# Optimization experiments

Hardware: AMD Instinct MI355X
Metric: run time of the kernel (lower is better)

Reference implementation:

```python
import jax, jax.numpy as jnp
import numpy as np

MIN_NORM = 1e-15
BALL_EPS_F32 = 0.004  # BALL_EPS[torch.float32]


def _norm(x):
    return jnp.maximum(jnp.linalg.norm(x, axis=-1, keepdims=True), MIN_NORM)


def project(x, c=1.0):
    norm = _norm(x)
    maxnorm = (1.0 - BALL_EPS_F32) / (c ** 0.5)
    return jnp.where(norm > maxnorm, x / norm * maxnorm, x)


def expmap0(u, c=1.0):
    sqrt_c = c ** 0.5
    un = _norm(u)
    gamma = jnp.tanh(jnp.clip(sqrt_c * un, -15.0, 15.0)) * u / (sqrt_c * un)
    return project(gamma, c)


def artanh(x):
    x = jnp.clip(x, -1.0 + 1e-5, 1.0 - 1e-5)
    return 0.5 * (jnp.log1p(x) - jnp.log1p(-x))


def logmap0(y, c=1.0):
    sqrt_c = c ** 0.5
    yn = _norm(y)
    return y / yn / sqrt_c * artanh(sqrt_c * yn)


def mobius_add(x, y, c=1.0):
    x2 = jnp.sum(x * x, axis=-1, keepdims=True)
    y2 = jnp.sum(y * y, axis=-1, keepdims=True)
    xy = jnp.sum(x * y, axis=-1, keepdims=True)
    num = (1 + 2 * c * xy + c * y2) * x + (1 - c * x2) * y
    denom = 1 + 2 * c * xy + (c ** 2) * x2 * y2
    return num / jnp.maximum(denom, MIN_NORM)


def p_exp_map(v):
    nv = jnp.maximum(jnp.linalg.norm(v, axis=-1, keepdims=True), 1e-10)
    return jnp.tanh(nv) * v / nv


def setup_inputs() -> dict:
    key = jax.random.key(0)
    ks = jax.random.split(key, 16)
    E, N, B = 1_000_000, 100_000, 512
    n_rel, D, A = 200, 64, 5
    R = 2 * n_rel + 1  # 401

    q_sub = jax.random.randint(ks[0], (B,), 0, N, dtype=jnp.int32)
    q_rel = jax.random.randint(ks[1], (B,), 0, R, dtype=jnp.int32)
    hidden = jax.random.normal(ks[2], (N, D), dtype=jnp.float32)

    r_idx = jax.random.randint(ks[3], (E,), 0, B, dtype=jnp.int32)
    rel = jax.random.randint(ks[4], (E,), 0, R, dtype=jnp.int32)
    sub = jax.random.randint(ks[5], (E,), 0, N, dtype=jnp.int32)
    obj = jax.random.randint(ks[6], (E,), 0, N, dtype=jnp.int32)
    dummy = jnp.zeros((E,), dtype=jnp.int32)
    edges = jnp.stack([r_idx, dummy, rel, dummy, sub, obj], axis=1)  # [E,6]

    s = 1.0 / np.sqrt(D)
    sa = 1.0 / np.sqrt(A)
    rela_embed = jax.random.normal(ks[7], (R, D), dtype=jnp.float32)
    query_embed = jax.random.normal(ks[8], (R, D), dtype=jnp.float32)
    Ws = jax.random.uniform(ks[9], (A, D), jnp.float32, -s, s)
    Wr = jax.random.uniform(ks[10], (A, D), jnp.float32, -s, s)
    Wqr_w = jax.random.uniform(ks[11], (A, D), jnp.float32, -s, s)
    Wqr_b = jax.random.uniform(ks[12], (A,), jnp.float32, -s, s)
    walpha_w = jax.random.uniform(ks[13], (1, A), jnp.float32, -sa, sa)
    walpha_b = jax.random.uniform(ks[14], (1,), jnp.float32, -sa, sa)
    Wh = jax.random.uniform(ks[15], (D, D), jnp.float32, -s, s)

    return {
        "q_sub": q_sub, "q_rel": q_rel, "hidden": hidden, "edges": edges,
        "n_node": N, "old_nodes_new_idx": jax.random.randint(jax.random.fold_in(key, 99), (100,), 0, N, dtype=jnp.int32),
        "rela_embed": rela_embed, "query_embed": query_embed,
        "Ws": Ws, "Wr": Wr, "Wqr_w": Wqr_w, "Wqr_b": Wqr_b,
        "walpha_w": walpha_w, "walpha_b": walpha_b, "Wh": Wh,
    }


def reference(q_sub, q_rel, hidden, edges, n_node, old_nodes_new_idx,
              rela_embed, query_embed, Ws, Wr, Wqr_w, Wqr_b,
              walpha_w, walpha_b, Wh):
    sub = edges[:, 4]
    rel = edges[:, 2]
    obj = edges[:, 5]
    r_idx = edges[:, 0]

    hs = hidden[sub]                     # [E, D] gather
    hr = rela_embed[rel]                 # [E, D]
    h_qr = query_embed[q_rel][r_idx]     # [E, D]

    # attention (note: bilinear/non_linear branch in the original is dead code)
    pre = hs @ Ws.T + hr @ Wr.T + (h_qr @ Wqr_w.T + Wqr_b)   # [E, A]
    alpha = jax.nn.sigmoid(jax.nn.relu(pre) @ walpha_w.T + walpha_b)  # [E, 1]

    hr_h = expmap0(hr, 1.0)
    hs_h = expmap0(hs, 1.0)
    message = logmap0(project(mobius_add(hs_h, hr_h, 1.0), 1.0), 1.0)
    message = alpha * message            # [E, D]

    message_agg = jax.ops.segment_sum(message, obj, num_segments=n_node)  # [N, D]
    a = message_agg @ Wh.T
    a = p_exp_map(a)
    hidden_new = logmap0(a, 1.0)         # act is identity
    return hidden_new
```

## Files before the change

kernel.cpp:

```cpp
#include <hip/hip_runtime.h>
#include <hip/hip_bf16.h>
#include <hip/hip_fp16.h>


__device__ __forceinline__ float wave_sum(float v) {
#pragma unroll
    for (int off = 32; off > 0; off >>= 1) v += __shfl_xor(v, off, 64);
    return v;
}

__device__ __forceinline__ float frcp(float x) {
#if __has_builtin(__builtin_amdgcn_rcpf)
    return __builtin_amdgcn_rcpf(x);
#else
    return 1.f / x;
#endif
}
__device__ __forceinline__ float fsqrt_(float x) {
#if __has_builtin(__builtin_amdgcn_sqrtf)
    return __builtin_amdgcn_sqrtf(x);
#else
    return sqrtf(x);
#endif
}
__device__ __forceinline__ float flog2_(float x) {
#if __has_builtin(__builtin_amdgcn_logf)
    return __builtin_amdgcn_logf(x);
#else
    return log2f(x);
#endif
}
__device__ __forceinline__ float fexp2_(float x) {
#if __has_builtin(__builtin_amdgcn_exp2f)
    return __builtin_amdgcn_exp2f(x);
#else
    return exp2f(x);
#endif
}

__device__ __forceinline__ unsigned pk2(float a, float b) {
    __half2 h = __floats2half2_rn(a, b);
    return __builtin_bit_cast(unsigned, h);
}
__device__ __forceinline__ float2 upk2(unsigned u) {
    __half2 h = __builtin_bit_cast(__half2, u);
    return __half22float2(h);
}

__device__ __forceinline__ void expmap0_scale(float norm, float& s, float& x2) {
    const float maxn = 1.0f - 0.004f;
    float un = fmaxf(norm, 1e-15f);
    float th = tanhf(fminf(un, 15.0f));
    float gs = th / un;
    float ng = gs * norm;
    float ps = ng > maxn ? maxn / ng : 1.0f;
    s = gs * ps;
    float sn = s * norm;
    x2 = sn * sn;
}


__global__ void prep_fused16(const int* __restrict__ q_rel,
                             const float* __restrict__ query_embed,
                             const float* __restrict__ Wqr_w,
                             const float* __restrict__ Wqr_b,
                             const float* __restrict__ rela_embed,
                             const float* __restrict__ Wr,
                             const float* __restrict__ hidden,
                             const float* __restrict__ Ws,
                             __half* __restrict__ hidden16,
                             uint4* __restrict__ hs_aux16,
                             __half* __restrict__ hr_h16,
                             uint4* __restrict__ hr_aux16,
                             uint4* __restrict__ preq16,
                             __half* __restrict__ agg16,
                             int N, int R, int B) {
    int wid = (blockIdx.x * blockDim.x + threadIdx.x) >> 6;
    int lane = threadIdx.x & 63;
    int nwaves = (N + 3) >> 2;
    if (wid < nwaves) {
        int q = lane >> 4, j = lane & 15;
        int n = wid * 4 + q;
        bool act = n < N;
        int nc = act ? n : N - 1;

        float4 u = *(const float4*)(hidden + (size_t)nc * 64 + 4 * j);
        float4 w0 = *(const float4*)(Ws + 0 * 64 + 4 * j);
        float4 w1 = *(const float4*)(Ws + 1 * 64 + 4 * j);
        float4 w2 = *(const float4*)(Ws + 2 * 64 + 4 * j);
        float4 w3 = *(const float4*)(Ws + 3 * 64 + 4 * j);
        float4 w4 = *(const float4*)(Ws + 4 * 64 + 4 * j);

#define DOT4(a, b) (fmaf((a).x, (b).x, fmaf((a).y, (b).y, fmaf((a).z, (b).z, (a).w * (b).w))))
        float p0 = DOT4(u, u);
        float p1 = DOT4(u, w0);
        float p2 = DOT4(u, w1);
        float p3 = DOT4(u, w2);
        float p4 = DOT4(u, w3);
        float p5 = DOT4(u, w4);
#undef DOT4
#pragma unroll
        for (int off = 1; off < 16; off <<= 1) {
            p0 += __shfl_xor(p0, off, 64);
            p1 += __shfl_xor(p1, off, 64);
            p2 += __shfl_xor(p2, off, 64);
            p3 += __shfl_xor(p3, off, 64);
            p4 += __shfl_xor(p4, off, 64);
            p5 += __shfl_xor(p5, off, 64);
        }
        float s, x2;
        expmap0_scale(fsqrt_(p0), s, x2);
        if (act) {
            uint2 hp; hp.x = pk2(u.x, u.y); hp.y = pk2(u.z, u.w);
            *(uint2*)(hidden16 + (size_t)n * 64 + 4 * j) = hp;
            uint2 zz; zz.x = 0u; zz.y = 0u;
            ((uint2*)(agg16 + (size_t)n * 64))[j] = zz;
            if (j == 0) {
                uint4 o; o.x = pk2(p1, p2); o.y = pk2(p3, p4); o.z = pk2(p5, 0.f); o.w = pk2(x2, s);
                hs_aux16[n] = o;
            }
        }
        return;
    }
    int w2 = wid - nwaves;
    if (w2 < R) {
        int r = w2;
        float u = rela_embed[r * 64 + lane];
        float p0 = u * u;
        float p1 = u * Wr[0 * 64 + lane];
        float p2 = u * Wr[1 * 64 + lane];
        float p3 = u * Wr[2 * 64 + lane];
        float p4 = u * Wr[3 * 64 + lane];
        float p5 = u * Wr[4 * 64 + lane];
#pragma unroll
        for (int off = 1; off < 64; off <<= 1) {
            p0 += __shfl_xor(p0, off, 64);
            p1 += __shfl_xor(p1, off, 64);
            p2 += __shfl_xor(p2, off, 64);
            p3 += __shfl_xor(p3, off, 64);
            p4 += __shfl_xor(p4, off, 64);
            p5 += __shfl_xor(p5, off, 64);
        }
        float s, y2;
        expmap0_scale(fsqrt_(p0), s, y2);
        hr_h16[r * 64 + lane] = __float2half(s * u);
        if (lane == 0) {
            uint4 o; o.x = pk2(p1, p2); o.y = pk2(p3, p4); o.z = pk2(p5, 0.f); o.w = pk2(y2, 0.f);
            hr_aux16[r] = o;
        }
    } else if (w2 < R + B) {
        int b = w2 - R;
        int qr = q_rel[b];
        float q = query_embed[qr * 64 + lane];
        float p1 = q * Wqr_w[0 * 64 + lane];
        float p2 = q * Wqr_w[1 * 64 + lane];
        float p3 = q * Wqr_w[2 * 64 + lane];
        float p4 = q * Wqr_w[3 * 64 + lane];
        float p5 = q * Wqr_w[4 * 64 + lane];
#pragma unroll
        for (int off = 1; off < 64; off <<= 1) {
            p1 += __shfl_xor(p1, off, 64);
            p2 += __shfl_xor(p2, off, 64);
            p3 += __shfl_xor(p3, off, 64);
            p4 += __shfl_xor(p4, off, 64);
            p5 += __shfl_xor(p5, off, 64);
        }
        if (lane == 0) {
            uint4 o;
            o.x = pk2(p1 + Wqr_b[0], p2 + Wqr_b[1]);
            o.y = pk2(p3 + Wqr_b[2], p4 + Wqr_b[3]);
            o.z = pk2(p5 + Wqr_b[4], 0.f);
            o.w = pk2(0.f, 0.f);
            preq16[b] = o;
        }
    }
}

__device__ __forceinline__ void edge_chain(
    unsigned hu_lo, unsigned hu_hi, unsigned yu_lo, unsigned yu_hi,
    uint4 hsa, uint4 hra, uint4 pqa,
    const float* wa, float wb,
    bool act, __half2* __restrict__ dst ) {
    float2 hs01 = upk2(hsa.x), hs23 = upk2(hsa.y), hs4 = upk2(hsa.z), hsxs = upk2(hsa.w);
    float2 hr01 = upk2(hra.x), hr23 = upk2(hra.y), hr4 = upk2(hra.z), hry = upk2(hra.w);
    float2 pq01 = upk2(pqa.x), pq23 = upk2(pqa.y), pq4 = upk2(pqa.z);
    float x2 = hsxs.x, s = hsxs.y, y2 = hry.x;

    float2 hl = upk2(hu_lo), hh = upk2(hu_hi);
    float2 yl = upk2(yu_lo), yh = upk2(yu_hi);

    float p = hl.x * yl.x;
    p = fmaf(hl.y, yl.y, p);
    p = fmaf(hh.x, yh.x, p);
    p = fmaf(hh.y, yh.y, p);
    p += __shfl_xor(p, 1, 64);
    p += __shfl_xor(p, 2, 64);
    p += __shfl_xor(p, 4, 64);
    p += __shfl_xor(p, 8, 64);
    float xy = p * s;

    float z = wb;
    z = fmaf(fmaxf(hs01.x + hr01.x + pq01.x, 0.f), wa[0], z);
    z = fmaf(fmaxf(hs01.y + hr01.y + pq01.y, 0.f), wa[1], z);
    z = fmaf(fmaxf(hs23.x + hr23.x + pq23.x, 0.f), wa[2], z);
    z = fmaf(fmaxf(hs23.y + hr23.y + pq23.y, 0.f), wa[3], z);
    z = fmaf(fmaxf(hs4.x + hr4.x + pq4.x, 0.f), wa[4], z);
    float alpha = frcp(1.f + fexp2_(z * -1.44269504f));

    float Af  = 1.f + 2.f * xy + y2;
    float Bf  = 1.f - x2;
    float den = fmaxf(1.f + 2.f * xy + x2 * y2, 1e-15f);
    float inv = frcp(den);
    float nm2 = fmaxf(fmaf(Af * Af, x2, fmaf(2.f * Af * Bf, xy, Bf * Bf * y2)), 0.f);
    float nm  = fsqrt_(nm2) * inv;
    const float maxn = 1.0f - 0.004f;
    float ps  = nm > maxn ? maxn * frcp(nm) : 1.f;
    float yn  = fmaxf(fminf(nm, maxn), 1e-15f);
    float ratio = (1.f + yn) * frcp(1.f - yn);
    float art = 0.34657359f * flog2_(ratio);
    float k  = inv * ps * alpha * art * frcp(yn);
    float cx = k * Af * s;
    float cy = k * Bf;

    __half2 q_lo = __floats2half2_rn(fmaf(cx, hl.x, cy * yl.x), fmaf(cx, hl.y, cy * yl.y));
    __half2 q_hi = __floats2half2_rn(fmaf(cx, hh.x, cy * yh.x), fmaf(cx, hh.y, cy * yh.y));
    if (act) {
        unsafeAtomicAdd(dst, q_lo);
        unsafeAtomicAdd(dst + 16, q_hi);
    }
}

__global__ __launch_bounds__(256) void edge_kernel8c(
    const int* __restrict__ edges,
    const __half* __restrict__ hidden16,
    const __half* __restrict__ hr_h16,
    const uint4* __restrict__ hs_aux16,
    const uint4* __restrict__ hr_aux16,
    const uint4* __restrict__ preq16,
    const float* __restrict__ walpha_w,
    const float* __restrict__ walpha_b,
    __half2* __restrict__ agg,
    int E)
{
    int wid = (blockIdx.x * blockDim.x + threadIdx.x) >> 6;
    int lane = threadIdx.x & 63;
    int g = lane >> 4;
    int j = lane & 15;

    int e0 = wid * 8 + g;
    int e1 = wid * 8 + 4 + g;
    bool act0 = e0 < E, act1 = e1 < E;
    int ec0 = act0 ? e0 : E - 1;
    int ec1 = act1 ? e1 : E - 1;

    const long long* er0 = (const long long*)(edges + (size_t)ec0 * 6);
    const long long* er1 = (const long long*)(edges + (size_t)ec1 * 6);
    long long a0 = __builtin_nontemporal_load(er0);
    long long b0 = __builtin_nontemporal_load(er0 + 1);
    long long c0 = __builtin_nontemporal_load(er0 + 2);
    long long a1 = __builtin_nontemporal_load(er1);
    long long b1 = __builtin_nontemporal_load(er1 + 1);
    long long c1 = __builtin_nontemporal_load(er1 + 2);
    int r0 = (int)a0, rel0 = (int)b0, sub0 = (int)c0, obj0 = (int)(c0 >> 32);
    int r1 = (int)a1, rel1 = (int)b1, sub1 = (int)c1, obj1 = (int)(c1 >> 32);

    uint4 hsa0 = hs_aux16[sub0];
    uint4 hra0 = hr_aux16[rel0];
    uint4 pqa0 = preq16[r0];
    uint4 hsa1 = hs_aux16[sub1];
    uint4 hra1 = hr_aux16[rel1];
    uint4 pqa1 = preq16[r1];

    const unsigned* hrow0 = (const unsigned*)(hidden16 + (size_t)sub0 * 64);
    const unsigned* yrow0 = (const unsigned*)(hr_h16 + (size_t)rel0 * 64);
    const unsigned* hrow1 = (const unsigned*)(hidden16 + (size_t)sub1 * 64);
    const unsigned* yrow1 = (const unsigned*)(hr_h16 + (size_t)rel1 * 64);
    unsigned hu_lo0 = hrow0[j], hu_hi0 = hrow0[16 + j];
    unsigned yu_lo0 = yrow0[j], yu_hi0 = yrow0[16 + j];
    unsigned hu_lo1 = hrow1[j], hu_hi1 = hrow1[16 + j];
    unsigned yu_lo1 = yrow1[j], yu_hi1 = yrow1[16 + j];

    float wa[5];
    wa[0] = walpha_w[0]; wa[1] = walpha_w[1]; wa[2] = walpha_w[2];
    wa[3] = walpha_w[3]; wa[4] = walpha_w[4];
    float wb = walpha_b[0];

    edge_chain(hu_lo0, hu_hi0, yu_lo0, yu_hi0, hsa0, hra0, pqa0, wa, wb,
               act0, agg + (size_t)obj0 * 32 + j);
    edge_chain(hu_lo1, hu_hi1, yu_lo1, yu_hi1, hsa1, hra1, pqa1, wa, wb,
               act1, agg + (size_t)obj1 * 32 + j);
}

__global__ __launch_bounds__(256) void final_gemm16(
    float* __restrict__ out,
    const __half* __restrict__ agg16,
    const float* __restrict__ Wh,
    int N)
{
    __shared__ __half tile[64 * 64];
    int t = threadIdx.x;
    int lane = t & 63;
    int w = t >> 6;

    float wh[64];
    const float4* whr = (const float4*)(Wh + (size_t)lane * 64);
#pragma unroll
    for (int i = 0; i < 16; ++i) {
        float4 v = whr[i];
        wh[4 * i] = v.x; wh[4 * i + 1] = v.y; wh[4 * i + 2] = v.z; wh[4 * i + 3] = v.w;
    }

    int ntiles = (N + 63) >> 6;
    for (int ti = blockIdx.x; ti < ntiles; ti += gridDim.x) {
        int base = ti << 6;
        int nrow = min(64, N - base);
        __syncthreads();
        {
            const uint2* src = (const uint2*)(agg16 + (size_t)base * 64);
            uint2* dst = (uint2*)tile;
            int nu2 = nrow * 16;
            for (int i = t; i < nu2; i += 256) dst[i] = src[i];
        }
        __syncthreads();
#pragma unroll 1
        for (int r = 0; r < 16; ++r) {
            int n = base + w * 16 + r;
            if (n >= N) break;
            const uint2* arow = (const uint2*)(tile + (w * 16 + r) * 64);
            float acc = 0.f;
#pragma unroll
            for (int kk = 0; kk < 16; ++kk) {
                uint2 u = arow[kk];
                float2 f0 = upk2(u.x), f1 = upk2(u.y);
                acc = fmaf(f0.x, wh[4 * kk], acc);
                acc = fmaf(f0.y, wh[4 * kk + 1], acc);
                acc = fmaf(f1.x, wh[4 * kk + 2], acc);
                acc = fmaf(f1.y, wh[4 * kk + 3], acc);
            }
            float n2 = wave_sum(acc * acc);
            float na = fsqrt_(n2);
            float nv = fmaxf(na, 1e-10f);
            float pn = tanhf(nv);
            float rinv = frcp(nv);
            float pp = pn * acc * rinv;
            float np = pn * (na * rinv);
            float yn = fmaxf(np, 1e-15f);
            float tt = fminf(yn, 1.f - 1e-5f);
            float ratio = (1.f + tt) * frcp(1.f - tt);
            float art = 0.34657359f * flog2_(ratio);
            out[(size_t)n * 64 + lane] = pp * art * frcp(yn);
        }
    }
}


__global__ void prep_small_kernel(const int* __restrict__ q_rel,
                                  const float* __restrict__ query_embed,
                                  const float* __restrict__ Wqr_w,
                                  const float* __restrict__ Wqr_b,
                                  const float* __restrict__ rela_embed,
                                  const float* __restrict__ Wr,
                                  float* __restrict__ hr_h,
                                  float* __restrict__ hr_aux,
                                  float* __restrict__ preq,
                                  int R, int B, int A) {
    int w = (blockIdx.x * blockDim.x + threadIdx.x) >> 6;
    int lane = threadIdx.x & 63;
    if (w < R) {
        int r = w;
        float u = rela_embed[r * 64 + lane];
        float n2 = wave_sum(u * u);
        float s, y2;
        expmap0_scale(fsqrt_(n2), s, y2);
        hr_h[r * 64 + lane] = s * u;
        for (int a = 0; a < A; ++a) {
            float p = wave_sum(u * Wr[a * 64 + lane]);
            if (lane == 0) hr_aux[r * 8 + a] = p;
        }
        if (lane == 0) hr_aux[r * 8 + 6] = y2;
    } else if (w < R + B) {
        int b = w - R;
        int qr = q_rel[b];
        float q = query_embed[qr * 64 + lane];
        for (int a = 0; a < A; ++a) {
            float p = wave_sum(q * Wqr_w[a * 64 + lane]);
            if (lane == 0) preq[b * 8 + a] = p + Wqr_b[a];
        }
    }
}

__global__ void prep_node_kernel(const float* __restrict__ hidden,
                                 const float* __restrict__ Ws,
                                 float* __restrict__ hs_aux, int N, int A) {
    int w = (blockIdx.x * blockDim.x + threadIdx.x) >> 6;
    if (w >= N) return;
    int lane = threadIdx.x & 63;
    float u = hidden[(size_t)w * 64 + lane];
    float n2 = wave_sum(u * u);
    float s, x2;
    expmap0_scale(fsqrt_(n2), s, x2);
    for (int a = 0; a < A; ++a) {
        float p = wave_sum(u * Ws[a * 64 + lane]);
        if (lane == 0) hs_aux[w * 8 + a] = p;
    }
    if (lane == 0) { hs_aux[w * 8 + 6] = x2; hs_aux[w * 8 + 7] = s; }
}

__global__ void edge_kernel_f32(const int* __restrict__ edges,
                                const float* __restrict__ hidden,
                                const float* __restrict__ hr_h,
                                const float* __restrict__ hr_aux,
                                const float* __restrict__ hs_aux,
                                const float* __restrict__ preq,
                                const float* __restrict__ walpha_w,
                                const float* __restrict__ walpha_b,
                                float* __restrict__ agg,
                                int E, int A) {
    int w = (blockIdx.x * blockDim.x + threadIdx.x) >> 6;
    if (w >= E) return;
    int lane = threadIdx.x & 63;
    const int* er = edges + (size_t)w * 6;
    int r_idx = er[0], rel = er[2], sub = er[4], obj = er[5];

    float s  = hs_aux[(size_t)sub * 8 + 7];
    float x2 = hs_aux[(size_t)sub * 8 + 6];
    float h  = hidden[(size_t)sub * 64 + lane];
    float x  = h * s;
    float y  = hr_h[(size_t)rel * 64 + lane];
    float y2 = hr_aux[(size_t)rel * 8 + 6];
    float xy = wave_sum(x * y);

    float z = walpha_b[0];
    for (int a = 0; a < A; ++a) {
        float pre = hs_aux[(size_t)sub * 8 + a] + hr_aux[(size_t)rel * 8 + a] + preq[(size_t)r_idx * 8 + a];
        z += fmaxf(pre, 0.f) * walpha_w[a];
    }
    float alpha = frcp(1.f + fexp2_(z * -1.44269504f));

    float Af = 1.f + 2.f * xy + y2;
    float Bf = 1.f - x2;
    float den = fmaxf(1.f + 2.f * xy + x2 * y2, 1e-15f);
    float inv = frcp(den);
    float nm2 = fmaxf(Af * Af * x2 + 2.f * Af * Bf * xy + Bf * Bf * y2, 0.f);
    float nm = fsqrt_(nm2) * inv;
    const float maxn = 1.0f - 0.004f;
    float ps = nm > maxn ? maxn * frcp(nm) : 1.f;
    float yn = fmaxf(fminf(nm, maxn), 1e-15f);
    float ratio = (1.f + yn) * frcp(1.f - yn);
    float art = 0.34657359f * flog2_(ratio);
    float k = inv * ps * alpha * art * frcp(yn);
    float msg = fmaf(k * Af * s, h, k * Bf * y);
    unsafeAtomicAdd(agg + (size_t)obj * 64 + lane, msg);
}

__global__ void final_kernel_f32(float* __restrict__ out,
                                 const float* __restrict__ Wh,
                                 int N) {
    __shared__ float WhT[64 * 64];
    int t = threadIdx.x;
    for (int i = t; i < 64 * 64; i += blockDim.x) {
        int row = i >> 6, col = i & 63;
        WhT[col * 64 + row] = Wh[i];
    }
    __syncthreads();

    int lane = t & 63;
    int wl = t >> 6;
    int wpb = blockDim.x >> 6;
    int wg = blockIdx.x * wpb + wl;
    int wstride = gridDim.x * wpb;

    for (int n = wg; n < N; n += wstride) {
        float v = out[(size_t)n * 64 + lane];
        float a = 0.f;
#pragma unroll
        for (int k = 0; k < 64; ++k)
            a = fmaf(__shfl(v, k, 64), WhT[k * 64 + lane], a);

        float n2 = wave_sum(a * a);
        float na = fsqrt_(n2);
        float nv = fmaxf(na, 1e-10f);
        float pn = tanhf(nv);
        float rinv = frcp(nv);
        float pp = pn * a * rinv;
        float np = pn * (na * rinv);
        float yn = fmaxf(np, 1e-15f);
        float tt = fminf(yn, 1.f - 1e-5f);
        float ratio = (1.f + tt) * frcp(1.f - tt);
        float art = 0.34657359f * flog2_(ratio);
        out[(size_t)n * 64 + lane] = pp * art * frcp(yn);
    }
}

extern "C" void kernel_launch(void* const* d_in, const int* in_sizes, int n_in,
                              void* d_out, int out_size, void* d_ws, size_t ws_size,
                              hipStream_t stream) {
    const int*   q_rel       = (const int*)d_in[1];
    const float* hidden      = (const float*)d_in[2];
    const int*   edges       = (const int*)d_in[3];
    const float* rela_embed  = (const float*)d_in[6];
    const float* query_embed = (const float*)d_in[7];
    const float* Ws          = (const float*)d_in[8];
    const float* Wr          = (const float*)d_in[9];
    const float* Wqr_w       = (const float*)d_in[10];
    const float* Wqr_b       = (const float*)d_in[11];
    const float* walpha_w    = (const float*)d_in[12];
    const float* walpha_b    = (const float*)d_in[13];
    const float* Wh          = (const float*)d_in[14];

    const int D = 64;
    int B = in_sizes[0];
    int E = in_sizes[3] / 6;
    int A = in_sizes[11];
    int R = in_sizes[6] / D;
    int N = out_size / D;

    float* out = (float*)d_out;

    size_t agg_b    = (size_t)N * 64 * 2;
    size_t hid16_b  = (size_t)N * 64 * 2;
    size_t hsaux_b  = (size_t)N * 16;
    size_t hrh_b    = (size_t)R * 64 * 2;
    size_t hraux_b  = (size_t)R * 16;
    size_t preq_b   = (size_t)B * 16;
    size_t need16   = agg_b + hid16_b + hsaux_b + hrh_b + hraux_b + preq_b;
    bool f16path = (A == 5) && (ws_size >= need16);

    if (f16path) {
        char* base = (char*)d_ws;
        __half2* agg      = (__half2*)base;                 base += agg_b;
        __half*  hidden16 = (__half*)base;                  base += hid16_b;
        uint4*   hs_aux16 = (uint4*)base;                   base += hsaux_b;
        __half*  hr_h16   = (__half*)base;                  base += hrh_b;
        uint4*   hr_aux16 = (uint4*)base;                   base += hraux_b;
        uint4*   preq16   = (uint4*)base;

        int nwaves = (N + 3) / 4;
        int total_waves = nwaves + R + B;
        prep_fused16<<<(total_waves + 3) / 4, 256, 0, stream>>>(
            q_rel, query_embed, Wqr_w, Wqr_b, rela_embed, Wr,
            hidden, Ws, hidden16, hs_aux16, hr_h16, hr_aux16, preq16,
            (__half*)agg, N, R, B);

        int ewaves = (E + 7) / 8;
        edge_kernel8c<<<(ewaves + 3) / 4, 256, 0, stream>>>(
            edges, hidden16, hr_h16, hs_aux16, hr_aux16, preq16,
            walpha_w, walpha_b, agg, E);

        final_gemm16<<<1024, 256, 0, stream>>>(out, (const __half*)agg, Wh, N);
    } else {
        float* hs_aux = (float*)d_ws;
        float* hr_h   = hs_aux + (size_t)N * 8;
        float* hr_aux = hr_h + (size_t)R * 64;
        float* preq   = hr_aux + (size_t)R * 8;

        hipMemsetAsync(d_out, 0, (size_t)out_size * sizeof(float), stream);

        int waves_small = R + B;
        prep_small_kernel<<<(waves_small * 64 + 255) / 256, 256, 0, stream>>>(
            q_rel, query_embed, Wqr_w, Wqr_b, rela_embed, Wr,
            hr_h, hr_aux, preq, R, B, A);

        prep_node_kernel<<<(N + 3) / 4, 256, 0, stream>>>(hidden, Ws, hs_aux, N, A);

        edge_kernel_f32<<<(E + 3) / 4, 256, 0, stream>>>(
            edges, hidden, hr_h, hr_aux, hs_aux, preq,
            walpha_w, walpha_b, out, E, A);

        final_kernel_f32<<<1024, 256, 0, stream>>>(out, Wh, N);
    }
}
```

Measured before the change: 161.7 us.

## Use exp2-based tanh, one tile per block in final GEMM, nontemporal output stores

Replaces tanhf with a fast exp2/rcp-based tanh for positive arguments in expmap0_scale and the final kernel, and uses rcp in place of divides. The final GEMM kernel drops its grid-stride loop, launches one block per 64-row tile, and writes the output with nontemporal stores. The edge kernel's helper is renamed and its loads are inlined at the call site, which should have no effect on speed. The trade-offs are some accuracy in tanh and the reciprocal, and extra per-block Wh loading because many more blocks are launched.

```diff
diff --git a/kernel.cpp b/kernel.cpp
--- a/kernel.cpp
+++ b/kernel.cpp
@@ -37,6 +37,9 @@
     return exp2f(x);
 #endif
 }
+__device__ __forceinline__ float ftanh_pos(float x) {
+    return 1.f - 2.f * frcp(fexp2_(x * 2.885390082f) + 1.f);
+}
 
 __device__ __forceinline__ unsigned pk2(float a, float b) {
     __half2 h = __floats2half2_rn(a, b);
@@ -50,15 +53,67 @@
 __device__ __forceinline__ void expmap0_scale(float norm, float& s, float& x2) {
     const float maxn = 1.0f - 0.004f;
     float un = fmaxf(norm, 1e-15f);
-    float th = tanhf(fminf(un, 15.0f));
-    float gs = th / un;
+    float th = ftanh_pos(fminf(un, 15.0f));
+    float gs = th * frcp(un);
     float ng = gs * norm;
-    float ps = ng > maxn ? maxn / ng : 1.0f;
+    float ps = ng > maxn ? maxn * frcp(ng) : 1.0f;
     s = gs * ps;
     float sn = s * norm;
     x2 = sn * sn;
 }
 
+__device__ __forceinline__ void edge_to_global(
+    unsigned hu_lo, unsigned hu_hi, unsigned yu_lo, unsigned yu_hi,
+    uint4 hsa, uint4 hra, uint4 pqa, const float* wa, float wb,
+    bool act, __half2* dst ) {
+    float2 hs01 = upk2(hsa.x), hs23 = upk2(hsa.y), hs4 = upk2(hsa.z), hsxs = upk2(hsa.w);
+    float2 hr01 = upk2(hra.x), hr23 = upk2(hra.y), hr4 = upk2(hra.z), hry = upk2(hra.w);
+    float2 pq01 = upk2(pqa.x), pq23 = upk2(pqa.y), pq4 = upk2(pqa.z);
+    float x2 = hsxs.x, s = hsxs.y, y2 = hry.x;
+
+    float2 hl = upk2(hu_lo), hh = upk2(hu_hi);
+    float2 yl = upk2(yu_lo), yh = upk2(yu_hi);
+
+    float p = hl.x * yl.x;
+    p = fmaf(hl.y, yl.y, p);
+    p = fmaf(hh.x, yh.x, p);
+    p = fmaf(hh.y, yh.y, p);
+    p += __shfl_xor(p, 1, 64);
+    p += __shfl_xor(p, 2, 64);
+    p += __shfl_xor(p, 4, 64);
+    p += __shfl_xor(p, 8, 64);
+    float xy = p * s;
+
+    float z = wb;
+    z = fmaf(fmaxf(hs01.x + hr01.x + pq01.x, 0.f), wa[0], z);
+    z = fmaf(fmaxf(hs01.y + hr01.y + pq01.y, 0.f), wa[1], z);
+    z = fmaf(fmaxf(hs23.x + hr23.x + pq23.x, 0.f), wa[2], z);
+    z = fmaf(fmaxf(hs23.y + hr23.y + pq23.y, 0.f), wa[3], z);
+    z = fmaf(fmaxf(hs4.x + hr4.x + pq4.x, 0.f), wa[4], z);
+    float alpha = frcp(1.f + fexp2_(z * -1.44269504f));
+
+    float Af  = 1.f + 2.f * xy + y2;
+    float Bf  = 1.f - x2;
+    float den = fmaxf(1.f + 2.f * xy + x2 * y2, 1e-15f);
+    float inv = frcp(den);
+    float nm2 = fmaxf(fmaf(Af * Af, x2, fmaf(2.f * Af * Bf, xy, Bf * Bf * y2)), 0.f);
+    float nm  = fsqrt_(nm2) * inv;
+    const float maxn = 1.0f - 0.004f;
+    float ps  = nm > maxn ? maxn * frcp(nm) : 1.f;
+    float yn  = fmaxf(fminf(nm, maxn), 1e-15f);
+    float ratio = (1.f + yn) * frcp(1.f - yn);
+    float art = 0.34657359f * flog2_(ratio);
+    float k  = inv * ps * alpha * art * frcp(yn);
+    float cx = k * Af * s;
+    float cy = k * Bf;
+
+    __half2 q_lo = __floats2half2_rn(fmaf(cx, hl.x, cy * yl.x), fmaf(cx, hl.y, cy * yl.y));
+    __half2 q_hi = __floats2half2_rn(fmaf(cx, hh.x, cy * yh.x), fmaf(cx, hh.y, cy * yh.y));
+    if (act) {
+        unsafeAtomicAdd(dst, q_lo);
+        unsafeAtomicAdd(dst + 16, q_hi);
+    }
+}
 
 __global__ void prep_fused16(const int* __restrict__ q_rel,
                              const float* __restrict__ query_embed,
@@ -176,60 +231,6 @@
     }
 }
 
-__device__ __forceinline__ void edge_chain(
-    unsigned hu_lo, unsigned hu_hi, unsigned yu_lo, unsigned yu_hi,
-    uint4 hsa, uint4 hra, uint4 pqa,
-    const float* wa, float wb,
-    bool act, __half2* __restrict__ dst ) {
-    float2 hs01 = upk2(hsa.x), hs23 = upk2(hsa.y), hs4 = upk2(hsa.z), hsxs = upk2(hsa.w);
-    float2 hr01 = upk2(hra.x), hr23 = upk2(hra.y), hr4 = upk2(hra.z), hry = upk2(hra.w);
-    float2 pq01 = upk2(pqa.x), pq23 = upk2(pqa.y), pq4 = upk2(pqa.z);
-    float x2 = hsxs.x, s = hsxs.y, y2 = hry.x;
-
-    float2 hl = upk2(hu_lo), hh = upk2(hu_hi);
-    float2 yl = upk2(yu_lo), yh = upk2(yu_hi);
-
-    float p = hl.x * yl.x;
-    p = fmaf(hl.y, yl.y, p);
-    p = fmaf(hh.x, yh.x, p);
-    p = fmaf(hh.y, yh.y, p);
-    p += __shfl_xor(p, 1, 64);
-    p += __shfl_xor(p, 2, 64);
-    p += __shfl_xor(p, 4, 64);
-    p += __shfl_xor(p, 8, 64);
-    float xy = p * s;
-
-    float z = wb;
-    z = fmaf(fmaxf(hs01.x + hr01.x + pq01.x, 0.f), wa[0], z);
-    z = fmaf(fmaxf(hs01.y + hr01.y + pq01.y, 0.f), wa[1], z);
-    z = fmaf(fmaxf(hs23.x + hr23.x + pq23.x, 0.f), wa[2], z);
-    z = fmaf(fmaxf(hs23.y + hr23.y + pq23.y, 0.f), wa[3], z);
-    z = fmaf(fmaxf(hs4.x + hr4.x + pq4.x, 0.f), wa[4], z);
-    float alpha = frcp(1.f + fexp2_(z * -1.44269504f));
-
-    float Af  = 1.f + 2.f * xy + y2;
-    float Bf  = 1.f - x2;
-    float den = fmaxf(1.f + 2.f * xy + x2 * y2, 1e-15f);
-    float inv = frcp(den);
-    float nm2 = fmaxf(fmaf(Af * Af, x2, fmaf(2.f * Af * Bf, xy, Bf * Bf * y2)), 0.f);
-    float nm  = fsqrt_(nm2) * inv;
-    const float maxn = 1.0f - 0.004f;
-    float ps  = nm > maxn ? maxn * frcp(nm) : 1.f;
-    float yn  = fmaxf(fminf(nm, maxn), 1e-15f);
-    float ratio = (1.f + yn) * frcp(1.f - yn);
-    float art = 0.34657359f * flog2_(ratio);
-    float k  = inv * ps * alpha * art * frcp(yn);
-    float cx = k * Af * s;
-    float cy = k * Bf;
-
-    __half2 q_lo = __floats2half2_rn(fmaf(cx, hl.x, cy * yl.x), fmaf(cx, hl.y, cy * yl.y));
-    __half2 q_hi = __floats2half2_rn(fmaf(cx, hh.x, cy * yh.x), fmaf(cx, hh.y, cy * yh.y));
-    if (act) {
-        unsafeAtomicAdd(dst, q_lo);
-        unsafeAtomicAdd(dst + 16, q_hi);
-    }
-}
-
 __global__ __launch_bounds__(256) void edge_kernel8c(
     const int* __restrict__ edges,
     const __half* __restrict__ hidden16,
@@ -264,31 +265,23 @@
     int r0 = (int)a0, rel0 = (int)b0, sub0 = (int)c0, obj0 = (int)(c0 >> 32);
     int r1 = (int)a1, rel1 = (int)b1, sub1 = (int)c1, obj1 = (int)(c1 >> 32);
 
-    uint4 hsa0 = hs_aux16[sub0];
-    uint4 hra0 = hr_aux16[rel0];
-    uint4 pqa0 = preq16[r0];
-    uint4 hsa1 = hs_aux16[sub1];
-    uint4 hra1 = hr_aux16[rel1];
-    uint4 pqa1 = preq16[r1];
+    uint4 hsa0 = hs_aux16[sub0], hra0 = hr_aux16[rel0], pqa0 = preq16[r0];
+    uint4 hsa1 = hs_aux16[sub1], hra1 = hr_aux16[rel1], pqa1 = preq16[r1];
 
     const unsigned* hrow0 = (const unsigned*)(hidden16 + (size_t)sub0 * 64);
     const unsigned* yrow0 = (const unsigned*)(hr_h16 + (size_t)rel0 * 64);
     const unsigned* hrow1 = (const unsigned*)(hidden16 + (size_t)sub1 * 64);
     const unsigned* yrow1 = (const unsigned*)(hr_h16 + (size_t)rel1 * 64);
-    unsigned hu_lo0 = hrow0[j], hu_hi0 = hrow0[16 + j];
-    unsigned yu_lo0 = yrow0[j], yu_hi0 = yrow0[16 + j];
-    unsigned hu_lo1 = hrow1[j], hu_hi1 = hrow1[16 + j];
-    unsigned yu_lo1 = yrow1[j], yu_hi1 = yrow1[16 + j];
 
     float wa[5];
     wa[0] = walpha_w[0]; wa[1] = walpha_w[1]; wa[2] = walpha_w[2];
     wa[3] = walpha_w[3]; wa[4] = walpha_w[4];
     float wb = walpha_b[0];
 
-    edge_chain(hu_lo0, hu_hi0, yu_lo0, yu_hi0, hsa0, hra0, pqa0, wa, wb,
-               act0, agg + (size_t)obj0 * 32 + j);
-    edge_chain(hu_lo1, hu_hi1, yu_lo1, yu_hi1, hsa1, hra1, pqa1, wa, wb,
-               act1, agg + (size_t)obj1 * 32 + j);
+    edge_to_global(hrow0[j], hrow0[16 + j], yrow0[j], yrow0[16 + j],
+                   hsa0, hra0, pqa0, wa, wb, act0, agg + (size_t)obj0 * 32 + j);
+    edge_to_global(hrow1[j], hrow1[16 + j], yrow1[j], yrow1[16 + j],
+                   hsa1, hra1, pqa1, wa, wb, act1, agg + (size_t)obj1 * 32 + j);
 }
 
 __global__ __launch_bounds__(256) void final_gemm16(
@@ -310,46 +303,43 @@
         wh[4 * i] = v.x; wh[4 * i + 1] = v.y; wh[4 * i + 2] = v.z; wh[4 * i + 3] = v.w;
     }
 
-    int ntiles = (N + 63) >> 6;
-    for (int ti = blockIdx.x; ti < ntiles; ti += gridDim.x) {
-        int base = ti << 6;
-        int nrow = min(64, N - base);
-        __syncthreads();
-        {
-            const uint2* src = (const uint2*)(agg16 + (size_t)base * 64);
-            uint2* dst = (uint2*)tile;
-            int nu2 = nrow * 16;
-            for (int i = t; i < nu2; i += 256) dst[i] = src[i];
-        }
-        __syncthreads();
+    int base = blockIdx.x << 6;
+    int nrow = min(64, N - base);
+    {
+        const uint2* src = (const uint2*)(agg16 + (size_t)base * 64);
+        uint2* dst = (uint2*)tile;
+        int nu2 = nrow * 16;
+        for (int i = t; i < nu2; i += 256) dst[i] = src[i];
+    }
+    __syncthreads();
+
 #pragma unroll 1
-        for (int r = 0; r < 16; ++r) {
-            int n = base + w * 16 + r;
-            if (n >= N) break;
-            const uint2* arow = (const uint2*)(tile + (w * 16 + r) * 64);
-            float acc = 0.f;
-#pragma unroll
-            for (int kk = 0; kk < 16; ++kk) {
-                uint2 u = arow[kk];
-                float2 f0 = upk2(u.x), f1 = upk2(u.y);
-                acc = fmaf(f0.x, wh[4 * kk], acc);
-                acc = fmaf(f0.y, wh[4 * kk + 1], acc);
-                acc = fmaf(f1.x, wh[4 * kk + 2], acc);
-                acc = fmaf(f1.y, wh[4 * kk + 3], acc);
-            }
-            float n2 = wave_sum(acc * acc);
-            float na = fsqrt_(n2);
-            float nv = fmaxf(na, 1e-10f);
-            float pn = tanhf(nv);
-            float rinv = frcp(nv);
-            float pp = pn * acc * rinv;
-            float np = pn * (na * rinv);
-            float yn = fmaxf(np, 1e-15f);
-            float tt = fminf(yn, 1.f - 1e-5f);
-            float ratio = (1.f + tt) * frcp(1.f - tt);
-            float art = 0.34657359f * flog2_(ratio);
-            out[(size_t)n * 64 + lane] = pp * art * frcp(yn);
-        }
+    for (int r = 0; r < 16; ++r) {
+        int n = base + w * 16 + r;
+        if (n >= N) break;
+        const uint2* arow = (const uint2*)(tile + (w * 16 + r) * 64);
+        float acc = 0.f;
+#pragma unroll
+        for (int kk = 0; kk < 16; ++kk) {
+            uint2 u = arow[kk];
+            float2 f0 = upk2(u.x), f1 = upk2(u.y);
+            acc = fmaf(f0.x, wh[4 * kk], acc);
+            acc = fmaf(f0.y, wh[4 * kk + 1], acc);
+            acc = fmaf(f1.x, wh[4 * kk + 2], acc);
+            acc = fmaf(f1.y, wh[4 * kk + 3], acc);
+        }
+        float n2 = wave_sum(acc * acc);
+        float na = fsqrt_(n2);
+        float nv = fmaxf(na, 1e-10f);
+        float pn = ftanh_pos(nv);
+        float rinv = frcp(nv);
+        float pp = pn * acc * rinv;
+        float np = pn * (na * rinv);
+        float yn = fmaxf(np, 1e-15f);
+        float tt = fminf(yn, 1.f - 1e-5f);
+        float ratio = (1.f + tt) * frcp(1.f - tt);
+        float art = 0.34657359f * flog2_(ratio);
+        __builtin_nontemporal_store(pp * art * frcp(yn), &out[(size_t)n * 64 + lane]);
     }
 }
 
@@ -517,10 +507,10 @@
 
     float* out = (float*)d_out;
 
-    size_t agg_b    = (size_t)N * 64 * 2;
-    size_t hid16_b  = (size_t)N * 64 * 2;
+    size_t agg_b    = (size_t)N * 128;
+    size_t hid16_b  = (size_t)N * 128;
     size_t hsaux_b  = (size_t)N * 16;
-    size_t hrh_b    = (size_t)R * 64 * 2;
+    size_t hrh_b    = (size_t)R * 128;
     size_t hraux_b  = (size_t)R * 16;
     size_t preq_b   = (size_t)B * 16;
     size_t need16   = agg_b + hid16_b + hsaux_b + hrh_b + hraux_b + preq_b;
@@ -528,11 +518,11 @@
 
     if (f16path) {
         char* base = (char*)d_ws;
-        __half2* agg      = (__half2*)base;                 base += agg_b;
-        __half*  hidden16 = (__half*)base;                  base += hid16_b;
-        uint4*   hs_aux16 = (uint4*)base;                   base += hsaux_b;
-        __half*  hr_h16   = (__half*)base;                  base += hrh_b;
-        uint4*   hr_aux16 = (uint4*)base;                   base += hraux_b;
+        __half2* agg      = (__half2*)base;          base += agg_b;
+        __half*  hidden16 = (__half*)base;           base += hid16_b;
+        uint4*   hs_aux16 = (uint4*)base;            base += hsaux_b;
+        __half*  hr_h16   = (__half*)base;           base += hrh_b;
+        uint4*   hr_aux16 = (uint4*)base;            base += hraux_b;
         uint4*   preq16   = (uint4*)base;
 
         int nwaves = (N + 3) / 4;
@@ -547,14 +537,15 @@
             edges, hidden16, hr_h16, hs_aux16, hr_aux16, preq16,
             walpha_w, walpha_b, agg, E);
 
-        final_gemm16<<<1024, 256, 0, stream>>>(out, (const __half*)agg, Wh, N);
+        int ntiles = (N + 63) / 64;
+        final_gemm16<<<ntiles, 256, 0, stream>>>(out, (const __half*)agg, Wh, N);
     } else {
         float* hs_aux = (float*)d_ws;
         float* hr_h   = hs_aux + (size_t)N * 8;
         float* hr_aux = hr_h + (size_t)R * 64;
         float* preq   = hr_aux + (size_t)R * 8;
 
-        hipMemsetAsync(d_out, 0, (size_t)out_size * sizeof(float), stream);
+        (void)hipMemsetAsync(d_out, 0, (size_t)out_size * sizeof(float), stream);
 
         int waves_small = R + B;
         prep_small_kernel<<<(waves_small * 64 + 255) / 256, 256, 0, stream>>>(
```

Result: faster. 157.1 us (-2.8%).
